# Performance work log

Measured on AMD Instinct MI355X. Metric: run time of the kernel, lower is better.

Reference implementation:

```python
import jax, jax.numpy as jnp
import numpy as np

K = 3  # kernel_size
PAD = 1


def _unfold3x3(x):
    # x: [b, c, h, w] -> patches [b, c, k*k, h, w] matching torch.nn.Unfold
    # ordering (row-major over the kernel window, channel outermost).
    b, c, h, w = x.shape
    xp = jnp.pad(x, ((0, 0), (0, 0), (PAD, PAD), (PAD, PAD)))
    patches = jnp.stack(
        [xp[:, :, i:i + h, j:j + w] for i in range(K) for j in range(K)],
        axis=2,
    )
    return patches  # [b, c, 9, h, w]


def setup_inputs() -> dict:
    key = jax.random.key(0)
    k1, k2, k3, k4 = jax.random.split(key, 4)
    b, c, h, w = 8, 64, 128, 128
    out_ch = 64
    x = jax.random.normal(k1, (b, c, h, w), dtype=jnp.float32)
    guide_ch = jax.random.normal(k2, (b, c, h, w), dtype=jnp.float32)
    guide_sp = jax.random.normal(k3, (b, K * K, h, w), dtype=jnp.float32)
    # kaiming_normal_ fan_out on [out, in, k^2, 1, 1]: fan_out = out * k^2 * 1 * 1?
    # torch fan_out for 5D conv weight = out_channels * receptive_field (k^2*1*1)
    fan_out = out_ch * (K * K)
    std = np.sqrt(2.0 / fan_out)
    weight = jax.random.normal(k4, (out_ch, c, K * K), dtype=jnp.float32) * std
    return {"x": x, "guide_ch": guide_ch, "guide_sp": guide_sp, "weight": weight}


def reference(x, guide_ch, guide_sp, weight):
    # filter: [b, c, k^2, h, w] = 1 + tanh(guide_ch[:, :, None] + guide_sp[:, None])
    filt = 1.0 + jnp.tanh(guide_ch[:, :, None, :, :] + guide_sp[:, None, :, :, :])
    patches = _unfold3x3(x)  # [b, c, 9, h, w]
    # conv3d with weight [out, in, k^2, 1, 1] == per-pixel reduction over (c, k^2)
    out = jnp.einsum('bckhw,ock->bohw', patches * filt, weight)
    return out
```

## Files before the change

kernel.cpp:

```cpp
#include <hip/hip_runtime.h>
#include <hip/hip_bf16.h>

typedef short short8 __attribute__((ext_vector_type(8)));
typedef float floatx4 __attribute__((ext_vector_type(4)));
typedef unsigned uint4v __attribute__((ext_vector_type(4)));

#define HWSZ 16384
#define WD 128
#define CD 64
#define OD 64
#define OSTR 132
#define XTROW (130 * 64)
#define WP_BYTES (9 * 64 * 64 * 2)
#define L2E2 2.8853900817779268f

__device__ __forceinline__ short f2bf(float f) {
    unsigned u = __builtin_bit_cast(unsigned, f);
    u += 0x7FFFu + ((u >> 16) & 1u);
    return (short)(u >> 16);
}

__device__ __forceinline__ unsigned pack2bf(float a, float b) {
    __hip_bfloat162 h = __float22bfloat162_rn(float2{a, b});
    unsigned u;
    __builtin_memcpy(&u, &h, 4);
    return u;
}

__device__ __forceinline__ float bf2f(short s) {
    return __builtin_bit_cast(float, ((unsigned)(unsigned short)s) << 16);
}

__global__ void prepack_w(const float* __restrict__ wgt, unsigned short* __restrict__ wp) {
    int idx = blockIdx.x * 256 + threadIdx.x;
    if (idx < 9 * 64 * 64) {
        int k = idx >> 12, o = (idx >> 6) & 63, c = idx & 63;
        wp[idx] = (unsigned short)f2bf(2.0f * wgt[o * 576 + c * 9 + k]);
    }
}

__global__ __launch_bounds__(256, 2)
void transpose_x(const float* __restrict__ x, unsigned short* __restrict__ xt) {
    __shared__ unsigned ld[128 * 33];
    const int tid = threadIdx.x;
    const int b = blockIdx.x >> 7;
    const int h = blockIdx.x & 127;
    const float* xr = x + (size_t)b * CD * HWSZ + h * WD;

    #pragma unroll
    for (int it = 0; it < 16; ++it) {
        int idx = it * 256 + tid;
        int cd = idx >> 7;
        int w  = idx & 127;
        float a  = xr[(size_t)(2 * cd) * HWSZ + w];
        float b2 = xr[(size_t)(2 * cd + 1) * HWSZ + w];
        ld[w * 33 + cd] = pack2bf(a, b2);
    }
    __syncthreads();

    unsigned short* xo = xt + (size_t)(b * 128 + h) * XTROW;
    if (tid < 16) {
        int slot = (tid >> 3) ? 129 : 0;
        int cq = tid & 7;
        *(uint4v*)&xo[slot * 64 + cq * 8] = (uint4v){0u, 0u, 0u, 0u};
    }
    #pragma unroll
    for (int it = 0; it < 4; ++it) {
        int idx = it * 256 + tid;
        int w = idx >> 3, cq = idx & 7;
        uint4v v;
        #pragma unroll
        for (int i = 0; i < 4; ++i) v[i] = ld[w * 33 + cq * 4 + i];
        *(uint4v*)&xo[(1 + w) * 64 + cq * 8] = v;
    }
}

__global__ __launch_bounds__(256, 4)
void paka_main(const float* __restrict__ gc, const float* __restrict__ gs,
               const unsigned short* __restrict__ wp,
               const unsigned short* __restrict__ xt, float* __restrict__ out)
{
    __shared__ float lo[64 * OSTR];

    const int tid  = threadIdx.x;
    const int wave = tid >> 6;
    const int lane = tid & 63;
    const int b = blockIdx.x >> 7;
    const int h = blockIdx.x & 127;

    const float* gcb = gc + (size_t)b * CD * HWSZ;
    const float* gsb = gs + (size_t)b * 9 * HWSZ;

    const int row = lane & 15;
    const int q   = lane >> 4;
    const int mt0 = wave * 2;

    float eg[2][2][8];
    #pragma unroll
    for (int mt = 0; mt < 2; ++mt) {
        int p = (mt0 + mt) * 16 + row;
        #pragma unroll
        for (int ks = 0; ks < 2; ++ks)
            #pragma unroll
            for (int j = 0; j < 8; ++j) {
                int c = ks * 32 + q * 8 + j;
                eg[mt][ks][j] = __builtin_amdgcn_exp2f(gcb[(size_t)c * HWSZ + h * WD + p] * L2E2);
            }
    }

    floatx4 acc[2][4];
    #pragma unroll
    for (int i = 0; i < 2; ++i)
        #pragma unroll
        for (int n = 0; n < 4; ++n)
            acc[i][n] = (floatx4){0.f, 0.f, 0.f, 0.f};

    #pragma unroll
    for (int dh = 0; dh < 3; ++dh) {
        const int hh = h + dh - 1;
        if ((unsigned)hh >= 128u) continue;

        const unsigned short* xr = xt + (size_t)(b * 128 + hh) * XTROW;

        float esd[3][2];
        #pragma unroll
        for (int dw = 0; dw < 3; ++dw)
            #pragma unroll
            for (int mt = 0; mt < 2; ++mt) {
                int p = (mt0 + mt) * 16 + row;
                esd[dw][mt] = __builtin_amdgcn_exp2f(gsb[(dh * 3 + dw) * HWSZ + h * WD + p] * L2E2);
            }

        #pragma unroll
        for (int dw = 0; dw < 3; ++dw) {
            const int k = dh * 3 + dw;
            #pragma unroll
            for (int ks = 0; ks < 2; ++ks) {
                short8 raw[2];
                #pragma unroll
                for (int mt = 0; mt < 2; ++mt) {
                    int wslot = (mt0 + mt) * 16 + row + dw;
                    raw[mt] = *(const short8*)&xr[(size_t)wslot * 64 + ks * 32 + q * 8];
                }
                short8 bv[4];
                #pragma unroll
                for (int nt = 0; nt < 4; ++nt)
                    bv[nt] = *(const short8*)&wp[k * 4096 + (nt * 16 + row) * 64 + ks * 32 + q * 8];

                short8 af[2];
                #pragma unroll
                for (int mt = 0; mt < 2; ++mt) {
                    float es = esd[dw][mt];
                    #pragma unroll
                    for (int jj = 0; jj < 4; ++jj) {
                        float d0 = fmaf(eg[mt][ks][2 * jj],     es, 1.0f);
                        float d1 = fmaf(eg[mt][ks][2 * jj + 1], es, 1.0f);
                        float r0 = __builtin_amdgcn_rcpf(d0);
                        float r1 = __builtin_amdgcn_rcpf(d1);
                        float x0 = bf2f(raw[mt][2 * jj]);
                        float x1 = bf2f(raw[mt][2 * jj + 1]);
                        float t0 = fmaf(-x0, r0, x0);
                        float t1 = fmaf(-x1, r1, x1);
                        ((unsigned*)&af[mt])[jj] = pack2bf(t0, t1);
                    }
                }
                #pragma unroll
                for (int nt = 0; nt < 4; ++nt) {
                    acc[0][nt] = __builtin_amdgcn_mfma_f32_16x16x32_bf16(af[0], bv[nt], acc[0][nt], 0, 0, 0);
                    acc[1][nt] = __builtin_amdgcn_mfma_f32_16x16x32_bf16(af[1], bv[nt], acc[1][nt], 0, 0, 0);
                }
            }
        }
    }

    #pragma unroll
    for (int i = 0; i < 2; ++i) {
        int prow = (mt0 + i) * 16 + q * 4;
        #pragma unroll
        for (int nt = 0; nt < 4; ++nt) {
            int o = nt * 16 + row;
            #pragma unroll
            for (int r = 0; r < 4; ++r)
                lo[o * OSTR + prow + r] = acc[i][nt][r];
        }
    }
    __syncthreads();

    float* outb = out + ((size_t)b * OD) * HWSZ + h * WD;
    #pragma unroll
    for (int it = 0; it < 8; ++it) {
        int idx = it * 256 + tid;
        int o = idx >> 5, p4 = (idx & 31) * 4;
        *(floatx4*)&outb[(size_t)o * HWSZ + p4] = *(const floatx4*)&lo[o * OSTR + p4];
    }
}

#define XSTR 72
__global__ __launch_bounds__(256, 3)
void paka_fallback(const float* __restrict__ x, const float* __restrict__ gc,
                   const float* __restrict__ gs, const float* __restrict__ wgt,
                   float* __restrict__ out)
{
    __shared__ union {
        struct { short xl[130 * XSTR]; short wl[3][64 * XSTR]; } s;
        float o[64 * OSTR];
    } lds;
    const int tid  = threadIdx.x;
    const int wave = tid >> 6;
    const int lane = tid & 63;
    const int b = blockIdx.x >> 7;
    const int h = blockIdx.x & 127;
    const float* xb  = x  + (size_t)b * CD * HWSZ;
    const float* gcb = gc + (size_t)b * CD * HWSZ;
    const float* gsb = gs + (size_t)b * 9 * HWSZ;
    const int row = lane & 15, q = lane >> 4, mt0 = wave * 2;
    float eg[2][2][8];
    #pragma unroll
    for (int mt = 0; mt < 2; ++mt) {
        int p = (mt0 + mt) * 16 + row;
        #pragma unroll
        for (int ks = 0; ks < 2; ++ks)
            #pragma unroll
            for (int j = 0; j < 8; ++j)
                eg[mt][ks][j] = __builtin_amdgcn_exp2f(gcb[(size_t)(ks * 32 + q * 8 + j) * HWSZ + h * WD + p] * L2E2);
    }
    float esv[9][2];
    #pragma unroll
    for (int k = 0; k < 9; ++k)
        #pragma unroll
        for (int mt = 0; mt < 2; ++mt)
            esv[k][mt] = __builtin_amdgcn_exp2f(gsb[k * HWSZ + h * WD + (mt0 + mt) * 16 + row] * L2E2);
    if (tid < 32) *(unsigned*)&lds.s.xl[0 * XSTR + tid * 2] = 0u;
    else if (tid < 64) *(unsigned*)&lds.s.xl[129 * XSTR + (tid - 32) * 2] = 0u;
    floatx4 acc[2][4];
    #pragma unroll
    for (int i = 0; i < 2; ++i)
        #pragma unroll
        for (int n = 0; n < 4; ++n) acc[i][n] = (floatx4){0.f, 0.f, 0.f, 0.f};
    #pragma unroll
    for (int dh = 0; dh < 3; ++dh) {
        const int hh = h + dh - 1;
        if ((unsigned)hh >= 128u) continue;
        __syncthreads();
        #pragma unroll
        for (int it = 0; it < 48; ++it) {
            int idx = it * 256 + tid;
            int dw = idx >> 12, o = (idx >> 6) & 63, c = idx & 63;
            lds.s.wl[dw][o * XSTR + c] = f2bf(wgt[o * 576 + c * 9 + dh * 3 + dw]);
        }
        #pragma unroll
        for (int it = 0; it < 4; ++it) {
            int idx = it * 256 + tid;
            int cp = idx >> 5, p4 = (idx & 31) * 4;
            const float* x0 = xb + (size_t)(2 * cp) * HWSZ + hh * WD + p4;
            floatx4 a = *(const floatx4*)x0;
            floatx4 c4 = *(const floatx4*)(x0 + HWSZ);
            #pragma unroll
            for (int i = 0; i < 4; ++i)
                *(unsigned*)&lds.s.xl[(p4 + i + 1) * XSTR + 2 * cp] = pack2bf(a[i], c4[i]);
        }
        __syncthreads();
        #pragma unroll
        for (int dw = 0; dw < 3; ++dw) {
            const int k = dh * 3 + dw;
            #pragma unroll
            for (int ks = 0; ks < 2; ++ks) {
                short8 af[2];
                #pragma unroll
                for (int mt = 0; mt < 2; ++mt) {
                    int wslot = (mt0 + mt) * 16 + row + dw;
                    short8 raw = *(const short8*)&lds.s.xl[wslot * XSTR + ks * 32 + q * 8];
                    float es = esv[k][mt];
                    #pragma unroll
                    for (int jj = 0; jj < 4; ++jj) {
                        float d0 = fmaf(eg[mt][ks][2 * jj],     es, 1.0f);
                        float d1 = fmaf(eg[mt][ks][2 * jj + 1], es, 1.0f);
                        float r0 = __builtin_amdgcn_rcpf(d0);
                        float r1 = __builtin_amdgcn_rcpf(d1);
                        float x20 = bf2f(raw[2 * jj]);     x20 += x20;
                        float x21 = bf2f(raw[2 * jj + 1]); x21 += x21;
                        float t0 = fmaf(-x20, r0, x20);
                        float t1 = fmaf(-x21, r1, x21);
                        ((unsigned*)&af[mt])[jj] = pack2bf(t0, t1);
                    }
                }
                #pragma unroll
                for (int nt = 0; nt < 4; ++nt) {
                    short8 bv = *(const short8*)&lds.s.wl[dw][(nt * 16 + row) * XSTR + ks * 32 + q * 8];
                    acc[0][nt] = __builtin_amdgcn_mfma_f32_16x16x32_bf16(af[0], bv, acc[0][nt], 0, 0, 0);
                    acc[1][nt] = __builtin_amdgcn_mfma_f32_16x16x32_bf16(af[1], bv, acc[1][nt], 0, 0, 0);
                }
            }
        }
    }
    __syncthreads();
    #pragma unroll
    for (int i = 0; i < 2; ++i) {
        int prow = (mt0 + i) * 16 + q * 4;
        #pragma unroll
        for (int nt = 0; nt < 4; ++nt) {
            int o = nt * 16 + row;
            #pragma unroll
            for (int r = 0; r < 4; ++r)
                lds.o[o * OSTR + prow + r] = acc[i][nt][r];
        }
    }
    __syncthreads();
    float* outb = out + ((size_t)b * OD) * HWSZ + h * WD;
    #pragma unroll
    for (int it = 0; it < 8; ++it) {
        int idx = it * 256 + tid;
        int o = idx >> 5, p4 = (idx & 31) * 4;
        *(floatx4*)&outb[(size_t)o * HWSZ + p4] = *(const floatx4*)&lds.o[o * OSTR + p4];
    }
}

extern "C" void kernel_launch(void* const* d_in, const int* in_sizes, int n_in,
                              void* d_out, int out_size, void* d_ws, size_t ws_size,
                              hipStream_t stream) {
    const float* x   = (const float*)d_in[0];
    const float* gcp = (const float*)d_in[1];
    const float* gsp = (const float*)d_in[2];
    const float* wgt = (const float*)d_in[3];
    float* out = (float*)d_out;

    const size_t xt_bytes = (size_t)8 * 128 * XTROW * 2;
    const size_t need = WP_BYTES + xt_bytes;
    if (ws_size >= need) {
        unsigned short* wp = (unsigned short*)d_ws;
        unsigned short* xt = (unsigned short*)((char*)d_ws + WP_BYTES);
        prepack_w<<<dim3(144), dim3(256), 0, stream>>>(wgt, wp);
        transpose_x<<<dim3(1024), dim3(256), 0, stream>>>(x, xt);
        paka_main<<<dim3(1024), dim3(256), 0, stream>>>(gcp, gsp, wp, xt, out);
    } else {
        paka_fallback<<<dim3(1024), dim3(256), 0, stream>>>(x, gcp, gsp, wgt, out);
    }
}
```

Before: 164.2 us.

## Split main kernel into single-wave blocks of 16 pixels, storing accumulators directly

Each block of paka_main now covers 16 pixels of one row with a single wave, where before it covered a full row with four waves, and the grid grows from 1024 to 8192 blocks. The LDS staging buffer and __syncthreads are removed, and MFMA accumulators are written straight to global memory as 16-byte stores. The intent is to raise occupancy and cut LDS and synchronisation overhead. In exchange, the weight fragments are reused across half as many pixel tiles per load, and the output stores are less coalesced (four floats per lane, strided by HWSZ).

After: 224.6 us. 1.37x slower.

```diff
diff --git a/kernel.cpp b/kernel.cpp
--- a/kernel.cpp
+++ b/kernel.cpp
@@ -75,45 +75,33 @@
     }
 }
 
-__global__ __launch_bounds__(256, 4)
+__global__ __launch_bounds__(64, 6)
 void paka_main(const float* __restrict__ gc, const float* __restrict__ gs,
                const unsigned short* __restrict__ wp,
                const unsigned short* __restrict__ xt, float* __restrict__ out)
 {
-    __shared__ float lo[64 * OSTR];
-
-    const int tid  = threadIdx.x;
-    const int wave = tid >> 6;
-    const int lane = tid & 63;
-    const int b = blockIdx.x >> 7;
-    const int h = blockIdx.x & 127;
-
-    const float* gcb = gc + (size_t)b * CD * HWSZ;
-    const float* gsb = gs + (size_t)b * 9 * HWSZ;
-
-    const int row = lane & 15;
-    const int q   = lane >> 4;
-    const int mt0 = wave * 2;
-
-    float eg[2][2][8];
-    #pragma unroll
-    for (int mt = 0; mt < 2; ++mt) {
-        int p = (mt0 + mt) * 16 + row;
-        #pragma unroll
-        for (int ks = 0; ks < 2; ++ks)
-            #pragma unroll
-            for (int j = 0; j < 8; ++j) {
-                int c = ks * 32 + q * 8 + j;
-                eg[mt][ks][j] = __builtin_amdgcn_exp2f(gcb[(size_t)c * HWSZ + h * WD + p] * L2E2);
-            }
-    }
-
-    floatx4 acc[2][4];
-    #pragma unroll
-    for (int i = 0; i < 2; ++i)
-        #pragma unroll
-        for (int n = 0; n < 4; ++n)
-            acc[i][n] = (floatx4){0.f, 0.f, 0.f, 0.f};
+    const int lane = threadIdx.x;
+    const int row  = lane & 15;
+    const int q    = lane >> 4;
+    const int idx  = blockIdx.x;
+    const int pt   = idx & 7;
+    const int h    = (idx >> 3) & 127;
+    const int b    = idx >> 10;
+    const int p    = pt * 16 + row;
+
+    const float* gcb = gc + (size_t)b * CD * HWSZ + h * WD + p;
+    const float* gsb = gs + (size_t)b * 9 * HWSZ + h * WD + p;
+
+    float eg[2][8];
+    #pragma unroll
+    for (int ks = 0; ks < 2; ++ks)
+        #pragma unroll
+        for (int j = 0; j < 8; ++j)
+            eg[ks][j] = __builtin_amdgcn_exp2f(gcb[(size_t)(ks * 32 + q * 8 + j) * HWSZ] * L2E2);
+
+    floatx4 acc[4];
+    #pragma unroll
+    for (int n = 0; n < 4; ++n) acc[n] = (floatx4){0.f, 0.f, 0.f, 0.f};
 
     #pragma unroll
     for (int dh = 0; dh < 3; ++dh) {
@@ -122,77 +110,44 @@
 
         const unsigned short* xr = xt + (size_t)(b * 128 + hh) * XTROW;
 
-        float esd[3][2];
+        float esd[3];
         #pragma unroll
         for (int dw = 0; dw < 3; ++dw)
-            #pragma unroll
-            for (int mt = 0; mt < 2; ++mt) {
-                int p = (mt0 + mt) * 16 + row;
-                esd[dw][mt] = __builtin_amdgcn_exp2f(gsb[(dh * 3 + dw) * HWSZ + h * WD + p] * L2E2);
-            }
+            esd[dw] = __builtin_amdgcn_exp2f(gsb[(size_t)(dh * 3 + dw) * HWSZ] * L2E2);
 
         #pragma unroll
         for (int dw = 0; dw < 3; ++dw) {
             const int k = dh * 3 + dw;
             #pragma unroll
             for (int ks = 0; ks < 2; ++ks) {
-                short8 raw[2];
-                #pragma unroll
-                for (int mt = 0; mt < 2; ++mt) {
-                    int wslot = (mt0 + mt) * 16 + row + dw;
-                    raw[mt] = *(const short8*)&xr[(size_t)wslot * 64 + ks * 32 + q * 8];
-                }
-                short8 bv[4];
-                #pragma unroll
-                for (int nt = 0; nt < 4; ++nt)
-                    bv[nt] = *(const short8*)&wp[k * 4096 + (nt * 16 + row) * 64 + ks * 32 + q * 8];
-
-                short8 af[2];
-                #pragma unroll
-                for (int mt = 0; mt < 2; ++mt) {
-                    float es = esd[dw][mt];
-                    #pragma unroll
-                    for (int jj = 0; jj < 4; ++jj) {
-                        float d0 = fmaf(eg[mt][ks][2 * jj],     es, 1.0f);
-                        float d1 = fmaf(eg[mt][ks][2 * jj + 1], es, 1.0f);
-                        float r0 = __builtin_amdgcn_rcpf(d0);
-                        float r1 = __builtin_amdgcn_rcpf(d1);
-                        float x0 = bf2f(raw[mt][2 * jj]);
-                        float x1 = bf2f(raw[mt][2 * jj + 1]);
-                        float t0 = fmaf(-x0, r0, x0);
-                        float t1 = fmaf(-x1, r1, x1);
-                        ((unsigned*)&af[mt])[jj] = pack2bf(t0, t1);
-                    }
+                short8 raw = *(const short8*)&xr[(size_t)(p + dw) * 64 + ks * 32 + q * 8];
+                short8 af;
+                float es = esd[dw];
+                #pragma unroll
+                for (int jj = 0; jj < 4; ++jj) {
+                    float d0 = fmaf(eg[ks][2 * jj],     es, 1.0f);
+                    float d1 = fmaf(eg[ks][2 * jj + 1], es, 1.0f);
+                    float r0 = __builtin_amdgcn_rcpf(d0);
+                    float r1 = __builtin_amdgcn_rcpf(d1);
+                    float x0 = bf2f(raw[2 * jj]);
+                    float x1 = bf2f(raw[2 * jj + 1]);
+                    float t0 = fmaf(-x0, r0, x0);
+                    float t1 = fmaf(-x1, r1, x1);
+                    ((unsigned*)&af)[jj] = pack2bf(t0, t1);
                 }
                 #pragma unroll
                 for (int nt = 0; nt < 4; ++nt) {
-                    acc[0][nt] = __builtin_amdgcn_mfma_f32_16x16x32_bf16(af[0], bv[nt], acc[0][nt], 0, 0, 0);
-                    acc[1][nt] = __builtin_amdgcn_mfma_f32_16x16x32_bf16(af[1], bv[nt], acc[1][nt], 0, 0, 0);
+                    short8 bv = *(const short8*)&wp[k * 4096 + (nt * 16 + row) * 64 + ks * 32 + q * 8];
+                    acc[nt] = __builtin_amdgcn_mfma_f32_16x16x32_bf16(af, bv, acc[nt], 0, 0, 0);
                 }
             }
         }
     }
 
-    #pragma unroll
-    for (int i = 0; i < 2; ++i) {
-        int prow = (mt0 + i) * 16 + q * 4;
-        #pragma unroll
-        for (int nt = 0; nt < 4; ++nt) {
-            int o = nt * 16 + row;
-            #pragma unroll
-            for (int r = 0; r < 4; ++r)
-                lo[o * OSTR + prow + r] = acc[i][nt][r];
-        }
-    }
-    __syncthreads();
-
-    float* outb = out + ((size_t)b * OD) * HWSZ + h * WD;
-    #pragma unroll
-    for (int it = 0; it < 8; ++it) {
-        int idx = it * 256 + tid;
-        int o = idx >> 5, p4 = (idx & 31) * 4;
-        *(floatx4*)&outb[(size_t)o * HWSZ + p4] = *(const floatx4*)&lo[o * OSTR + p4];
-    }
+    float* ob = out + (size_t)b * OD * HWSZ + h * WD + pt * 16 + q * 4;
+    #pragma unroll
+    for (int nt = 0; nt < 4; ++nt)
+        *(floatx4*)&ob[(size_t)(nt * 16 + row) * HWSZ] = acc[nt];
 }
 
 #define XSTR 72
@@ -331,7 +286,7 @@
         unsigned short* xt = (unsigned short*)((char*)d_ws + WP_BYTES);
         prepack_w<<<dim3(144), dim3(256), 0, stream>>>(wgt, wp);
         transpose_x<<<dim3(1024), dim3(256), 0, stream>>>(x, xt);
-        paka_main<<<dim3(1024), dim3(256), 0, stream>>>(gcp, gsp, wp, xt, out);
+        paka_main<<<dim3(8192), dim3(64), 0, stream>>>(gcp, gsp, wp, xt, out);
     } else {
         paka_fallback<<<dim3(1024), dim3(256), 0, stream>>>(x, gcp, gsp, wgt, out);
     }
```

## Flatten tap loop with prefetched x loads, masked boundary rows, and direct output stores

Applied to the files above, without the earlier changes.

Replaces the nested dh/dw/ks loop with a flat 18-step loop that double-buffers the next step's x-tile load from global memory. Boundary rows now use clamped pointers and a zero multiplier on the spatial exp factor instead of skipping taps. All guide loads are issued up front before the exp2 pass. The LDS transpose and barrier for the output are removed; each lane stores its MFMA accumulator directly as float4. This aims to hide load latency and drop the epilogue sync, at the cost of more registers, always running all nine taps, and less coalesced output writes.

Result: no change. 164.7 us (+0.3%).

```diff
diff --git a/kernel.cpp b/kernel.cpp
--- a/kernel.cpp
+++ b/kernel.cpp
@@ -80,33 +80,63 @@
                const unsigned short* __restrict__ wp,
                const unsigned short* __restrict__ xt, float* __restrict__ out)
 {
-    __shared__ float lo[64 * OSTR];
-
     const int tid  = threadIdx.x;
     const int wave = tid >> 6;
     const int lane = tid & 63;
+    const int row  = lane & 15;
+    const int q    = lane >> 4;
+    const int qo   = q * 8;
     const int b = blockIdx.x >> 7;
     const int h = blockIdx.x & 127;
 
-    const float* gcb = gc + (size_t)b * CD * HWSZ;
-    const float* gsb = gs + (size_t)b * 9 * HWSZ;
-
-    const int row = lane & 15;
-    const int q   = lane >> 4;
-    const int mt0 = wave * 2;
+    const int p0 = wave * 32 + row;
+    const int p1 = p0 + 16;
+
+    const float* gcb = gc + (size_t)b * CD * HWSZ + h * WD;
+    const float* gsb = gs + (size_t)b * 9 * HWSZ + h * WD;
+
+    const unsigned short* xrp[3];
+    float rmask[3];
+    #pragma unroll
+    for (int dh = 0; dh < 3; ++dh) {
+        int hh = h + dh - 1;
+        rmask[dh] = ((unsigned)hh < 128u) ? 1.0f : 0.0f;
+        int hc = hh < 0 ? 0 : (hh > 127 ? 127 : hh);
+        xrp[dh] = xt + (size_t)(b * 128 + hc) * XTROW;
+    }
 
     float eg[2][2][8];
     #pragma unroll
     for (int mt = 0; mt < 2; ++mt) {
-        int p = (mt0 + mt) * 16 + row;
+        int p = mt ? p1 : p0;
         #pragma unroll
         for (int ks = 0; ks < 2; ++ks)
             #pragma unroll
-            for (int j = 0; j < 8; ++j) {
-                int c = ks * 32 + q * 8 + j;
-                eg[mt][ks][j] = __builtin_amdgcn_exp2f(gcb[(size_t)c * HWSZ + h * WD + p] * L2E2);
-            }
-    }
+            for (int j = 0; j < 8; ++j)
+                eg[mt][ks][j] = gcb[(size_t)(ks * 32 + qo + j) * HWSZ + p];
+    }
+    float esv[9][2];
+    #pragma unroll
+    for (int k = 0; k < 9; ++k) {
+        esv[k][0] = gsb[(size_t)k * HWSZ + p0];
+        esv[k][1] = gsb[(size_t)k * HWSZ + p1];
+    }
+    short8 rawv[2][2];
+    rawv[0][0] = *(const short8*)&xrp[0][(size_t)p0 * 64 + qo];
+    rawv[0][1] = *(const short8*)&xrp[0][(size_t)p1 * 64 + qo];
+
+    #pragma unroll
+    for (int mt = 0; mt < 2; ++mt)
+        #pragma unroll
+        for (int ks = 0; ks < 2; ++ks)
+            #pragma unroll
+            for (int j = 0; j < 8; ++j)
+                eg[mt][ks][j] = __builtin_amdgcn_exp2f(eg[mt][ks][j] * L2E2);
+    #pragma unroll
+    for (int k = 0; k < 9; ++k)
+        #pragma unroll
+        for (int mt = 0; mt < 2; ++mt)
+            esv[k][mt] = __builtin_amdgcn_exp2f(esv[k][mt] * L2E2) * rmask[k / 3];
 
     floatx4 acc[2][4];
     #pragma unroll
@@ -116,83 +146,53 @@
             acc[i][n] = (floatx4){0.f, 0.f, 0.f, 0.f};
 
     #pragma unroll
-    for (int dh = 0; dh < 3; ++dh) {
-        const int hh = h + dh - 1;
-        if ((unsigned)hh >= 128u) continue;
-
-        const unsigned short* xr = xt + (size_t)(b * 128 + hh) * XTROW;
-
-        float esd[3][2];
-        #pragma unroll
-        for (int dw = 0; dw < 3; ++dw)
-            #pragma unroll
-            for (int mt = 0; mt < 2; ++mt) {
-                int p = (mt0 + mt) * 16 + row;
-                esd[dw][mt] = __builtin_amdgcn_exp2f(gsb[(dh * 3 + dw) * HWSZ + h * WD + p] * L2E2);
+    for (int s = 0; s < 18; ++s) {
+        const int k  = s >> 1;
+        const int ks = s & 1;
+
+        if (s + 1 < 18) {
+            const int s1 = s + 1;
+            const int dh1 = s1 / 6, dw1 = (s1 >> 1) % 3, ks1 = s1 & 1;
+            rawv[s1 & 1][0] = *(const short8*)&xrp[dh1][(size_t)(p0 + dw1) * 64 + ks1 * 32 + qo];
+            rawv[s1 & 1][1] = *(const short8*)&xrp[dh1][(size_t)(p1 + dw1) * 64 + ks1 * 32 + qo];
+        }
+
+        short8 bv[4];
+        #pragma unroll
+        for (int nt = 0; nt < 4; ++nt)
+            bv[nt] = *(const short8*)&wp[k * 4096 + (nt * 16 + row) * 64 + ks * 32 + qo];
+
+        short8 af[2];
+        #pragma unroll
+        for (int mt = 0; mt < 2; ++mt) {
+            const float es = esv[k][mt];
+            const short8 raw = rawv[s & 1][mt];
+            #pragma unroll
+            for (int jj = 0; jj < 4; ++jj) {
+                float d0 = fmaf(eg[mt][ks][2 * jj],     es, 1.0f);
+                float d1 = fmaf(eg[mt][ks][2 * jj + 1], es, 1.0f);
+                float r0 = __builtin_amdgcn_rcpf(d0);
+                float r1 = __builtin_amdgcn_rcpf(d1);
+                float x0 = bf2f(raw[2 * jj]);
+                float x1 = bf2f(raw[2 * jj + 1]);
+                float t0 = fmaf(-x0, r0, x0);
+                float t1 = fmaf(-x1, r1, x1);
+                ((unsigned*)&af[mt])[jj] = pack2bf(t0, t1);
             }
-
-        #pragma unroll
-        for (int dw = 0; dw < 3; ++dw) {
-            const int k = dh * 3 + dw;
-            #pragma unroll
-            for (int ks = 0; ks < 2; ++ks) {
-                short8 raw[2];
-                #pragma unroll
-                for (int mt = 0; mt < 2; ++mt) {
-                    int wslot = (mt0 + mt) * 16 + row + dw;
-                    raw[mt] = *(const short8*)&xr[(size_t)wslot * 64 + ks * 32 + q * 8];
-                }
-                short8 bv[4];
-                #pragma unroll
-                for (int nt = 0; nt < 4; ++nt)
-                    bv[nt] = *(const short8*)&wp[k * 4096 + (nt * 16 + row) * 64 + ks * 32 + q * 8];
-
-                short8 af[2];
-                #pragma unroll
-                for (int mt = 0; mt < 2; ++mt) {
-                    float es = esd[dw][mt];
-                    #pragma unroll
-                    for (int jj = 0; jj < 4; ++jj) {
-                        float d0 = fmaf(eg[mt][ks][2 * jj],     es, 1.0f);
-                        float d1 = fmaf(eg[mt][ks][2 * jj + 1], es, 1.0f);
-                        float r0 = __builtin_amdgcn_rcpf(d0);
-                        float r1 = __builtin_amdgcn_rcpf(d1);
-                        float x0 = bf2f(raw[mt][2 * jj]);
-                        float x1 = bf2f(raw[mt][2 * jj + 1]);
-                        float t0 = fmaf(-x0, r0, x0);
-                        float t1 = fmaf(-x1, r1, x1);
-                        ((unsigned*)&af[mt])[jj] = pack2bf(t0, t1);
-                    }
-                }
-                #pragma unroll
-                for (int nt = 0; nt < 4; ++nt) {
-                    acc[0][nt] = __builtin_amdgcn_mfma_f32_16x16x32_bf16(af[0], bv[nt], acc[0][nt], 0, 0, 0);
-                    acc[1][nt] = __builtin_amdgcn_mfma_f32_16x16x32_bf16(af[1], bv[nt], acc[1][nt], 0, 0, 0);
-                }
-            }
-        }
-    }
-
-    #pragma unroll
-    for (int i = 0; i < 2; ++i) {
-        int prow = (mt0 + i) * 16 + q * 4;
+        }
         #pragma unroll
         for (int nt = 0; nt < 4; ++nt) {
-            int o = nt * 16 + row;
-            #pragma unroll
-            for (int r = 0; r < 4; ++r)
-                lo[o * OSTR + prow + r] = acc[i][nt][r];
-        }
-    }
-    __syncthreads();
-
-    float* outb = out + ((size_t)b * OD) * HWSZ + h * WD;
-    #pragma unroll
-    for (int it = 0; it < 8; ++it) {
-        int idx = it * 256 + tid;
-        int o = idx >> 5, p4 = (idx & 31) * 4;
-        *(floatx4*)&outb[(size_t)o * HWSZ + p4] = *(const floatx4*)&lo[o * OSTR + p4];
-    }
+            acc[0][nt] = __builtin_amdgcn_mfma_f32_16x16x32_bf16(af[0], bv[nt], acc[0][nt], 0, 0, 0);
+            acc[1][nt] = __builtin_amdgcn_mfma_f32_16x16x32_bf16(af[1], bv[nt], acc[1][nt], 0, 0, 0);
+        }
+    }
+
+    float* ob = out + (size_t)b * OD * HWSZ + h * WD + q * 4;
+    #pragma unroll
+    for (int mt = 0; mt < 2; ++mt)
+        #pragma unroll
+        for (int nt = 0; nt < 4; ++nt)
+            *(floatx4*)&ob[(size_t)(nt * 16 + row) * HWSZ + (wave * 2 + mt) * 16] = acc[mt][nt];
 }
 
 #define XSTR 72
```
